# Kernel optimization log

Measured on AMD Instinct MI355X. Metric: run time of the kernel, lower is better.

## Reference

```python
import jax, jax.numpy as jnp
import numpy as np

T, B, F = 160, 640, 40          # time-major input [T, B, F]
H, PJ, L = 768, 256, 3          # nb_hidden, nb_proj, nb_layers
FORGET_BIAS = 1.0               # TF LSTMCell default


def _glorot(k, shape):
    std = (2.0 / (shape[0] + shape[1])) ** 0.5
    return jax.random.normal(k, shape, jnp.float32) * std


def setup_inputs() -> dict:
    key = jax.random.key(0)
    ks = jax.random.split(key, 7)
    x = jax.random.normal(ks[0], (T, B, F), jnp.float32)
    # layer 0: input dim F + proj state PJ; layers 1,2: input dim PJ + PJ
    W0 = _glorot(ks[1], (F + PJ, 4 * H)); b0 = jnp.zeros((4 * H,), jnp.float32)
    P0 = _glorot(ks[2], (H, PJ))
    W1 = _glorot(ks[3], (PJ + PJ, 4 * H)); b1 = jnp.zeros((4 * H,), jnp.float32)
    P1 = _glorot(ks[4], (H, PJ))
    W2 = _glorot(ks[5], (PJ + PJ, 4 * H)); b2 = jnp.zeros((4 * H,), jnp.float32)
    P2 = _glorot(ks[6], (H, PJ))
    return {"x": x, "W0": W0, "b0": b0, "P0": P0,
            "W1": W1, "b1": b1, "P1": P1,
            "W2": W2, "b2": b2, "P2": P2}


def _cell(xt, c, h, W, b, P):
    # TF LSTMCell with num_proj: gates on [x, m_prev]; gate order i, j, f, o.
    z = jnp.concatenate([xt, h], axis=-1) @ W + b            # [B, 4H]
    i, j, f, o = jnp.split(z, 4, axis=-1)
    c_new = jax.nn.sigmoid(f + FORGET_BIAS) * c + jax.nn.sigmoid(i) * jnp.tanh(j)
    m = jax.nn.sigmoid(o) * jnp.tanh(c_new)                  # [B, H]
    h_new = m @ P                                            # projected state [B, PJ]
    return c_new, h_new


def reference(x, W0, b0, P0, W1, b1, P1, W2, b2, P2):
    params = ((W0, b0, P0), (W1, b1, P1), (W2, b2, P2))
    Bd = x.shape[1]
    init = tuple((jnp.zeros((Bd, H), x.dtype), jnp.zeros((Bd, PJ), x.dtype))
                 for _ in range(L))

    def step(carry, xt):
        inp = xt
        new = []
        for (c, h), (W, b, P) in zip(carry, params):
            c, h = _cell(inp, c, h, W, b, P)
            new.append((c, h))
            inp = h
        return tuple(new), None

    carry, _ = jax.lax.scan(step, init, x)
    emb = carry[-1][1]                                       # last layer h at final step, [B, PJ]
    # tf.nn.l2_normalize
    return emb / jnp.sqrt(jnp.maximum(jnp.sum(emb * emb, axis=-1, keepdims=True), 1e-12))
```

## Files before the change

kernel.cpp:

```cpp
#include <hip/hip_runtime.h>

#define Bdim 640
#define Hdim 768
#define PJdim 256
#define Tdim 160
#define NSTEP (Tdim + 2)

typedef _Float16 half8 __attribute__((ext_vector_type(8)));
typedef float floatx4 __attribute__((ext_vector_type(4)));

constexpr size_t HB_HALFS = 3ull * Bdim * PJdim;
constexpr size_t ZP_OFF   = HB_HALFS * 2;
constexpr size_t MB_OFF   = ZP_OFF + 256;
constexpr size_t MB_HALFS = 3ull * Bdim * Hdim;
constexpr size_t X_OFF    = MB_OFF + MB_HALFS * 2;
constexpr size_t X_HALFS  = (size_t)Tdim * Bdim * 40;
constexpr size_t W_OFF    = X_OFF + X_HALFS * 2;
constexpr size_t W_HALFS  = 36ull * 131072;
constexpr size_t P_OFF    = W_OFF + W_HALFS * 2;
constexpr size_t P_HALFS  = 3ull * 196608;
constexpr size_t C_OFF    = P_OFF + P_HALFS * 2;
constexpr size_t C_BYTES  = 3ull * Bdim * Hdim * 4;

__device__ __forceinline__ float sigm(float v) { return 1.0f / (1.0f + __expf(-v)); }
__device__ __forceinline__ float tanh_fast(float v) { return 2.0f / (1.0f + __expf(-2.0f * v)) - 1.0f; }

__device__ __forceinline__ void st_coh16b(void* p, _Float16 h) {
    union { _Float16 h; unsigned short u; } cv; cv.h = h;
    __hip_atomic_store((unsigned short*)p, cv.u, __ATOMIC_RELAXED, __HIP_MEMORY_SCOPE_AGENT);
}

__device__ __forceinline__ void pipe_wait(unsigned* c0, unsigned t0, unsigned* c1, unsigned t1)
{
    if (threadIdx.x == 0) {
        if (t0)
            while (__hip_atomic_load(c0, __ATOMIC_RELAXED, __HIP_MEMORY_SCOPE_AGENT) < t0)
                __builtin_amdgcn_s_sleep(1);
        if (c1 && t1)
            while (__hip_atomic_load(c1, __ATOMIC_RELAXED, __HIP_MEMORY_SCOPE_AGENT) < t1)
                __builtin_amdgcn_s_sleep(1);
        __builtin_amdgcn_fence(__ATOMIC_ACQUIRE, "agent");
    }
    __syncthreads();
}

__device__ __forceinline__ void pipe_sig(unsigned* c)
{
    __syncthreads();
    if (threadIdx.x == 0)
        __hip_atomic_fetch_add(c, 1u, __ATOMIC_RELAXED, __HIP_MEMORY_SCOPE_AGENT);
}

__global__ void repack_kernel(const float* __restrict__ x,
                              const float* __restrict__ W0, const float* __restrict__ W1,
                              const float* __restrict__ W2, const float* __restrict__ P0,
                              const float* __restrict__ P1, const float* __restrict__ P2,
                              _Float16* __restrict__ Wfrag, _Float16* __restrict__ Pfrag,
                              _Float16* __restrict__ x16)
{
    size_t idx = (size_t)blockIdx.x * 256 + threadIdx.x;
    if (idx < W_HALFS) {
        int slab = (int)(idx >> 17);
        int l = slab / 12, ht = slab % 12;
        int r  = (int)(idx & 131071);
        int kc = r >> 13;
        int r2 = r & 8191;
        int g  = r2 >> 11;
        int cf = (r2 >> 9) & 3;
        int u  = r2 & 511;
        int lane = u >> 3, e = u & 7;
        int qd = lane >> 4, ln = lane & 15;
        int k   = kc * 32 + qd * 8 + e;
        int col = g * Hdim + ht * 64 + cf * 16 + ln;
        float v;
        if (l == 0)      v = (k < 296) ? W0[(size_t)k * 3072 + col] : 0.0f;
        else if (l == 1) v = W1[(size_t)k * 3072 + col];
        else             v = W2[(size_t)k * 3072 + col];
        Wfrag[idx] = (_Float16)v;
    } else if (idx < W_HALFS + P_HALFS) {
        size_t i = idx - W_HALFS;
        int l = (int)(i / 196608);
        int r = (int)(i % 196608);
        int cq = r / 49152;
        int r2 = r % 49152;
        int kc = r2 / 2048;
        int r3 = r2 & 2047;
        int cgr = r3 >> 9;
        int u  = r3 & 511;
        int lane = u >> 3, e = u & 7;
        int qd = lane >> 4, ln = lane & 15;
        int k  = kc * 32 + qd * 8 + e;
        int pj = cq * 64 + cgr * 16 + ln;
        const float* P = (l == 0) ? P0 : (l == 1) ? P1 : P2;
        Pfrag[i] = (_Float16)P[(size_t)k * PJdim + pj];
    } else if (idx < W_HALFS + P_HALFS + X_HALFS) {
        size_t i = idx - W_HALFS - P_HALFS;
        x16[i] = (_Float16)x[i];
    }
}

__device__ __forceinline__ void gate_step(
    int l, int b0r, int h0, int KC, int t,
    const half8 (&Breg)[16][2], float (&c)[8][2],
    const float (&bia)[2], const float (&bja)[2], const float (&bfa)[2], const float (&boa)[2],
    const _Float16* __restrict__ x16, const _Float16* __restrict__ h16,
    const _Float16* __restrict__ zerop, _Float16* __restrict__ mbuf,
    _Float16* __restrict__ Ast, float* __restrict__ zst, int tid)
{
    const int wv = tid >> 6, lane = tid & 63, qd = lane >> 4, ln = lane & 15;
    const int g = wv >> 1, hh = wv & 1;
    const int qd8 = qd * 8;
    const int rowg = b0r + wv * 16 + ln;

    const _Float16* xt  = x16 + ((size_t)t * Bdim + rowg) * 40;
    const _Float16* h0b = h16 + (size_t)rowg * PJdim - 40;
    const _Float16* lob = (l > 0) ? h16 + ((size_t)(l - 1) * Bdim + rowg) * PJdim : nullptr;
    const _Float16* hib = h16 + ((size_t)l * Bdim + rowg) * PJdim - 256;

    auto srcp = [&](int kc) -> const _Float16* {
        int k = kc * 32 + qd8;
        if (l == 0) return (k < 40) ? xt + k : (k < 296) ? h0b + k : zerop;
        return (k < 256) ? lob + k : hib + k;
    };

    floatx4 acc[8][2];
    const floatx4 fz = {0.f, 0.f, 0.f, 0.f};
#pragma unroll
    for (int i = 0; i < 8; ++i) { acc[i][0] = fz; acc[i][1] = fz; }

    const int CH = KC >> 1;
    uint4 pre0 = *(const uint4*)srcp(0);
    uint4 pre1 = *(const uint4*)srcp(1);
#pragma unroll
    for (int ch = 0; ch < 8; ++ch) {
        if (ch < CH) {
            _Float16* Aw = Ast + (size_t)(ch & 1) * 8192 + wv * 512 + lane * 8;
            *(uint4*)Aw          = pre0;
            *(uint4*)(Aw + 4096) = pre1;
            if (ch + 1 < CH) {
                pre0 = *(const uint4*)srcp(2 * ch + 2);
                pre1 = *(const uint4*)srcp(2 * ch + 3);
            }
            __syncthreads();
            const _Float16* Ab = Ast + (size_t)(ch & 1) * 8192;
#pragma unroll
            for (int sub = 0; sub < 2; ++sub)
#pragma unroll
                for (int rf = 0; rf < 8; ++rf) {
                    half8 af = *(const half8*)(Ab + sub * 4096 + rf * 512 + lane * 8);
                    acc[rf][0] = __builtin_amdgcn_mfma_f32_16x16x32_f16(af, Breg[2 * ch + sub][0], acc[rf][0], 0, 0, 0);
                    acc[rf][1] = __builtin_amdgcn_mfma_f32_16x16x32_f16(af, Breg[2 * ch + sub][1], acc[rf][1], 0, 0, 0);
                }
        }
    }

    const int trow = tid >> 5;
    const int hc0  = (tid * 2) & 63;
#pragma unroll
    for (int rf = 0; rf < 8; ++rf) {
        __syncthreads();
#pragma unroll
        for (int cf = 0; cf < 2; ++cf)
#pragma unroll
            for (int r = 0; r < 4; ++r)
                zst[(qd * 4 + r) * 256 + g * 64 + hh * 32 + cf * 16 + ln] = acc[rf][cf][r];
        __syncthreads();
        _Float16 mh[2];
#pragma unroll
        for (int j = 0; j < 2; ++j) {
            int hc = hc0 + j;
            float zi = zst[trow * 256 + hc]       + bia[j];
            float zj = zst[trow * 256 + 64 + hc]  + bja[j];
            float zf = zst[trow * 256 + 128 + hc] + bfa[j];
            float zo = zst[trow * 256 + 192 + hc] + boa[j];
            float cn = sigm(zf) * c[rf][j] + sigm(zi) * tanh_fast(zj);
            c[rf][j] = cn;
            mh[j] = (_Float16)(sigm(zo) * tanh_fast(cn));
        }
        union { _Float16 h2[2]; unsigned u; } pk;
        pk.h2[0] = mh[0]; pk.h2[1] = mh[1];
        int row_g = b0r + rf * 16 + trow;
        *(unsigned*)(mbuf + ((size_t)l * Bdim + row_g) * Hdim + h0 + hc0) = pk.u;
    }
}

__device__ __forceinline__ void proj_step(
    int l, int b0r, int cq, const half8 (&Preg)[24],
    const _Float16* __restrict__ mbuf, _Float16* __restrict__ h16,
    _Float16* __restrict__ Ast, int tid, bool xstore)
{
    const int wv = tid >> 6, lane = tid & 63, qd = lane >> 4, ln = lane & 15;
    const int rh = wv >> 2, cgi = wv & 3;
    const int rowg = b0r + wv * 16 + ln;
    const _Float16* mrow = mbuf + ((size_t)l * Bdim + rowg) * Hdim + qd * 8;

    floatx4 pacc[4];
    const floatx4 fz = {0.f, 0.f, 0.f, 0.f};
#pragma unroll
    for (int i = 0; i < 4; ++i) pacc[i] = fz;

    uint4 pre0 = *(const uint4*)(mrow);
    uint4 pre1 = *(const uint4*)(mrow + 32);
#pragma unroll
    for (int ch = 0; ch < 12; ++ch) {
        _Float16* Aw = Ast + (size_t)(ch & 1) * 8192 + wv * 512 + lane * 8;
        *(uint4*)Aw          = pre0;
        *(uint4*)(Aw + 4096) = pre1;
        if (ch < 11) {
            pre0 = *(const uint4*)(mrow + (2 * ch + 2) * 32);
            pre1 = *(const uint4*)(mrow + (2 * ch + 3) * 32);
        }
        __syncthreads();
        const _Float16* Ab = Ast + (size_t)(ch & 1) * 8192;
#pragma unroll
        for (int sub = 0; sub < 2; ++sub)
#pragma unroll
            for (int rfl = 0; rfl < 4; ++rfl) {
                half8 af = *(const half8*)(Ab + sub * 4096 + (rh * 4 + rfl) * 512 + lane * 8);
                pacc[rfl] = __builtin_amdgcn_mfma_f32_16x16x32_f16(af, Preg[2 * ch + sub], pacc[rfl], 0, 0, 0);
            }
    }
    if (xstore) {
#pragma unroll
        for (int rfl = 0; rfl < 4; ++rfl)
#pragma unroll
            for (int r = 0; r < 4; ++r) {
                int row = b0r + (rh * 4 + rfl) * 16 + qd * 4 + r;
                st_coh16b(h16 + ((size_t)l * Bdim + row) * PJdim + cq * 64 + cgi * 16 + ln,
                          (_Float16)pacc[rfl][r]);
            }
    } else {
#pragma unroll
        for (int rfl = 0; rfl < 4; ++rfl)
#pragma unroll
            for (int r = 0; r < 4; ++r) {
                int row = b0r + (rh * 4 + rfl) * 16 + qd * 4 + r;
                h16[((size_t)l * Bdim + row) * PJdim + cq * 64 + cgi * 16 + ln] = (_Float16)pacc[rfl][r];
            }
    }
}

__device__ __forceinline__ void load_Breg(const _Float16* __restrict__ Wfrag, int l, int ht,
                                          int wv, int lane, half8 (&Breg)[16][2])
{
    const int g = wv >> 1, hh = wv & 1;
    const _Float16* wslab = Wfrag + ((size_t)(l * 12 + ht)) * 131072;
#pragma unroll
    for (int kc = 0; kc < 16; ++kc)
#pragma unroll
        for (int cf = 0; cf < 2; ++cf)
            Breg[kc][cf] = *(const half8*)(wslab + kc * 8192 + g * 2048 + (hh * 2 + cf) * 512 + lane * 8);
}

__device__ __forceinline__ void load_Preg(const _Float16* __restrict__ Pfrag, int l, int cq,
                                          int wv, int lane, half8 (&Preg)[24])
{
    const int cgi = wv & 3;
    const _Float16* pslab = Pfrag + (size_t)l * 196608 + (size_t)cq * 49152;
#pragma unroll
    for (int kc = 0; kc < 24; ++kc)
        Preg[kc] = *(const half8*)(pslab + kc * 2048 + cgi * 512 + lane * 8);
}

__device__ __forceinline__ void load_bias(const float* __restrict__ bias, int h0, int tid,
                                          float (&bia)[2], float (&bja)[2], float (&bfa)[2], float (&boa)[2])
{
    int hcg = h0 + ((tid * 2) & 63);
#pragma unroll
    for (int j = 0; j < 2; ++j) {
        bia[j] = bias[hcg + j];
        bja[j] = bias[Hdim + hcg + j];
        bfa[j] = bias[2 * Hdim + hcg + j] + 1.0f;
        boa[j] = bias[3 * Hdim + hcg + j];
    }
}

__device__ __forceinline__ void finalize_row(const _Float16* __restrict__ h16,
                                             float* __restrict__ out, int row, int lane)
{
    const _Float16* e = h16 + ((size_t)2 * Bdim + row) * PJdim + lane * 4;
    float v0 = (float)e[0], v1 = (float)e[1], v2 = (float)e[2], v3 = (float)e[3];
    float ss = v0 * v0 + v1 * v1 + v2 * v2 + v3 * v3;
#pragma unroll
    for (int o = 32; o > 0; o >>= 1) ss += __shfl_xor(ss, o, 64);
    float rs = rsqrtf(fmaxf(ss, 1e-12f));
    float4 o4; o4.x = v0 * rs; o4.y = v1 * rs; o4.z = v2 * rs; o4.w = v3 * rs;
    *(float4*)(out + (size_t)row * PJdim + lane * 4) = o4;
}

__global__ __launch_bounds__(512)
void lstm_persist(const _Float16* __restrict__ x16, const _Float16* __restrict__ Wfrag,
                  const _Float16* __restrict__ Pfrag,
                  const float* __restrict__ bias0, const float* __restrict__ bias1,
                  const float* __restrict__ bias2,
                  _Float16* __restrict__ h16, _Float16* __restrict__ mbuf,
                  const _Float16* __restrict__ zerop, float* __restrict__ out,
                  unsigned* __restrict__ flags)
{
    __shared__ __align__(16) _Float16 Ast[2 * 8192];
    __shared__ __align__(16) float zst[16 * 256];

    const int tid = threadIdx.x, bid = blockIdx.x;
    const int wv = tid >> 6, lane = tid & 63;

    const int xcd = bid & 7, slot = bid >> 3;
    const int gid = xcd * 2 + (slot >> 4);
    const int rr  = slot & 15;
    if (gid >= 15) return;
    const int bt2 = gid / 3, l = gid % 3;
    const int b0r = bt2 * 128;

    unsigned* gd = flags + (size_t)gid * 64;
    unsigned* pd = gd + 32;

    if (rr < 12) {
        const int ht = rr, h0 = ht * 64;
        const int KC = (l == 0) ? 10 : 16;
        half8 Breg[16][2];
        load_Breg(Wfrag, l, ht, wv, lane, Breg);
        float bia[2], bja[2], bfa[2], boa[2];
        load_bias((l == 0) ? bias0 : (l == 1) ? bias1 : bias2, h0, tid, bia, bja, bfa, boa);
        float c[8][2];
#pragma unroll
        for (int i = 0; i < 8; ++i) { c[i][0] = 0.f; c[i][1] = 0.f; }
        unsigned* pd_lo = (l > 0) ? flags + (size_t)(gid - 1) * 64 + 32 : nullptr;
        for (int t = 0; t < Tdim; ++t) {
            pipe_wait(pd, 4u * (unsigned)t, pd_lo, (l > 0) ? 4u * (unsigned)(t + 1) : 0u);
            gate_step(l, b0r, h0, KC, t, Breg, c, bia, bja, bfa, boa,
                      x16, h16, zerop, mbuf, Ast, zst, tid);
            pipe_sig(gd);
        }
        if (l == 2 && rr < 8) {
            pipe_wait(pd, 4u * (unsigned)Tdim, nullptr, 0u);
            int row0 = b0r + rr * 16 + wv * 2;
            finalize_row(h16, out, row0, lane);
            finalize_row(h16, out, row0 + 1, lane);
        }
    } else {
        const int cq = rr - 12;
        const bool xstore = ((gid & 1) == 1) && (gid + 1 < 15) && ((gid + 1) % 3 != 0);
        half8 Preg[24];
        load_Preg(Pfrag, l, cq, wv, lane, Preg);
        unsigned* gd_hi = (l < 2) ? flags + (size_t)(gid + 1) * 64 : nullptr;
        for (int t = 0; t < Tdim; ++t) {
            pipe_wait(gd, 12u * (unsigned)(t + 1), gd_hi, (l < 2) ? 12u * (unsigned)t : 0u);
            proj_step(l, b0r, cq, Preg, mbuf, h16, Ast, tid, xstore);
            pipe_sig(pd);
        }
    }
}

__global__ __launch_bounds__(512)
void gate_fb(const _Float16* __restrict__ x16, const _Float16* __restrict__ Wfrag,
             const float* __restrict__ bias0, const float* __restrict__ bias1,
             const float* __restrict__ bias2,
             _Float16* __restrict__ h16, _Float16* __restrict__ mbuf,
             const _Float16* __restrict__ zerop, float* __restrict__ cfb, int s)
{
    __shared__ __align__(16) _Float16 Ast[2 * 8192];
    __shared__ __align__(16) float zst[16 * 256];
    const int tid = threadIdx.x, bid = blockIdx.x;
    const int ht = bid % 12, z = bid / 12, l = z % 3, bt2 = z / 3;
    const int t = s - l;
    if (t < 0 || t >= Tdim) return;
    const int wv = tid >> 6, lane = tid & 63;
    const int b0r = bt2 * 128, h0 = ht * 64;
    const int KC = (l == 0) ? 10 : 16;
    half8 Breg[16][2];
    load_Breg(Wfrag, l, ht, wv, lane, Breg);
    float bia[2], bja[2], bfa[2], boa[2];
    load_bias((l == 0) ? bias0 : (l == 1) ? bias1 : bias2, h0, tid, bia, bja, bfa, boa);
    const int trow = tid >> 5, hc0 = (tid * 2) & 63;
    float c[8][2];
#pragma unroll
    for (int rf = 0; rf < 8; ++rf)
#pragma unroll
        for (int j = 0; j < 2; ++j)
            c[rf][j] = cfb[((size_t)l * Bdim + b0r + rf * 16 + trow) * Hdim + h0 + hc0 + j];
    gate_step(l, b0r, h0, KC, t, Breg, c, bia, bja, bfa, boa, x16, h16, zerop, mbuf, Ast, zst, tid);
#pragma unroll
    for (int rf = 0; rf < 8; ++rf)
#pragma unroll
        for (int j = 0; j < 2; ++j)
            cfb[((size_t)l * Bdim + b0r + rf * 16 + trow) * Hdim + h0 + hc0 + j] = c[rf][j];
}

__global__ __launch_bounds__(512)
void proj_fb(const _Float16* __restrict__ Pfrag, const _Float16* __restrict__ mbuf,
             _Float16* __restrict__ h16, int s)
{
    __shared__ __align__(16) _Float16 Ast[2 * 8192];
    const int tid = threadIdx.x, bid = blockIdx.x;
    const int cq = bid & 3, z = bid >> 2, l = z % 3, bt2 = z / 3;
    const int tp = s - l;
    if (tp < 0 || tp >= Tdim) return;
    const int wv = tid >> 6, lane = tid & 63;
    half8 Preg[24];
    load_Preg(Pfrag, l, cq, wv, lane, Preg);
    proj_step(l, bt2 * 128, cq, Preg, mbuf, h16, Ast, tid, false);
}

__global__ __launch_bounds__(512)
void fin_fb(const _Float16* __restrict__ h16, float* __restrict__ out)
{
    int row = blockIdx.x * 8 + (threadIdx.x >> 6);
    finalize_row(h16, out, row, threadIdx.x & 63);
}

extern "C" void kernel_launch(void* const* d_in, const int* in_sizes, int n_in,
                              void* d_out, int out_size, void* d_ws, size_t ws_size,
                              hipStream_t stream)
{
    (void)in_sizes; (void)n_in; (void)out_size; (void)ws_size;
    const float* x  = (const float*)d_in[0];
    const float* W0 = (const float*)d_in[1];
    const float* b0 = (const float*)d_in[2];
    const float* P0 = (const float*)d_in[3];
    const float* W1 = (const float*)d_in[4];
    const float* b1 = (const float*)d_in[5];
    const float* P1 = (const float*)d_in[6];
    const float* W2 = (const float*)d_in[7];
    const float* b2 = (const float*)d_in[8];
    const float* P2 = (const float*)d_in[9];

    char* ws = (char*)d_ws;
    _Float16* h16   = (_Float16*)(ws);
    _Float16* zerop = (_Float16*)(ws + ZP_OFF);
    _Float16* mbuf  = (_Float16*)(ws + MB_OFF);
    _Float16* x16   = (_Float16*)(ws + X_OFF);
    _Float16* Wfrag = (_Float16*)(ws + W_OFF);
    _Float16* Pfrag = (_Float16*)(ws + P_OFF);
    float*    cfb   = (float*)(ws + C_OFF);
    unsigned* flags = (unsigned*)(ws + C_OFF);
    float*    outp  = (float*)d_out;

    hipMemsetAsync(ws, 0, ZP_OFF + 256, stream);
    hipMemsetAsync(cfb, 0, C_BYTES, stream);

    {
        constexpr size_t total = W_HALFS + P_HALFS + X_HALFS;
        int grid = (int)((total + 255) / 256);
        repack_kernel<<<grid, 256, 0, stream>>>(x, W0, W1, W2, P0, P1, P2, Wfrag, Pfrag, x16);
    }

    int occ = 0;
    hipError_t oe = hipOccupancyMaxActiveBlocksPerMultiprocessor(&occ, lstm_persist, 512, 0);
    bool coop = (oe == hipSuccess && occ >= 1);
    if (coop) {
        void* args[] = { (void*)&x16, (void*)&Wfrag, (void*)&Pfrag,
                         (void*)&b0, (void*)&b1, (void*)&b2,
                         (void*)&h16, (void*)&mbuf, (void*)&zerop, (void*)&outp,
                         (void*)&flags };
        hipError_t le = hipLaunchCooperativeKernel((const void*)lstm_persist,
                                                   dim3(256), dim3(512), args, 0, stream);
        if (le != hipSuccess) { (void)hipGetLastError(); coop = false; }
    }
    if (!coop) {
        for (int s = 0; s < NSTEP; ++s) {
            gate_fb<<<180, 512, 0, stream>>>(x16, Wfrag, b0, b1, b2, h16, mbuf, zerop, cfb, s);
            proj_fb<<<60, 512, 0, stream>>>(Pfrag, mbuf, h16, s);
        }
        fin_fb<<<80, 512, 0, stream>>>(h16, outp);
    }
}
```

Before: 4.766 ms.

## Batch LDS staging into large K chunks and vectorize gate epilogue

The gate and projection GEMM loops now stage eight K-chunks of activations into shared memory at once, instead of double-buffering two chunks per barrier. This cuts the number of __syncthreads per step from about 8–12 down to 2–4. The gate epilogue stages four row-fragments at a time into a larger zst buffer and processes 8 contiguous hidden units per thread with float4 loads. Biases move to shared memory, and mbuf writes become 16-byte stores. The cost is much larger LDS use (about 64KB zst plus 64KB Ast) and more registers held for prefetch, which may reduce occupancy or change the overlap of loads with MFMA.

```diff
diff --git a/kernel.cpp b/kernel.cpp
--- a/kernel.cpp
+++ b/kernel.cpp
@@ -101,11 +101,11 @@
 
 __device__ __forceinline__ void gate_step(
     int l, int b0r, int h0, int KC, int t,
-    const half8 (&Breg)[16][2], float (&c)[8][2],
-    const float (&bia)[2], const float (&bja)[2], const float (&bfa)[2], const float (&boa)[2],
+    const half8 (&Breg)[16][2], float (&c)[2][8],
     const _Float16* __restrict__ x16, const _Float16* __restrict__ h16,
     const _Float16* __restrict__ zerop, _Float16* __restrict__ mbuf,
-    _Float16* __restrict__ Ast, float* __restrict__ zst, int tid)
+    _Float16* __restrict__ Ast, float* __restrict__ zst, const float* __restrict__ bst,
+    int tid)
 {
     const int wv = tid >> 6, lane = tid & 63, qd = lane >> 4, ln = lane & 15;
     const int g = wv >> 1, hh = wv & 1;
@@ -128,59 +128,84 @@
 #pragma unroll
     for (int i = 0; i < 8; ++i) { acc[i][0] = fz; acc[i][1] = fz; }
 
-    const int CH = KC >> 1;
-    uint4 pre0 = *(const uint4*)srcp(0);
-    uint4 pre1 = *(const uint4*)srcp(1);
-#pragma unroll
-    for (int ch = 0; ch < 8; ++ch) {
-        if (ch < CH) {
-            _Float16* Aw = Ast + (size_t)(ch & 1) * 8192 + wv * 512 + lane * 8;
-            *(uint4*)Aw          = pre0;
-            *(uint4*)(Aw + 4096) = pre1;
-            if (ch + 1 < CH) {
-                pre0 = *(const uint4*)srcp(2 * ch + 2);
-                pre1 = *(const uint4*)srcp(2 * ch + 3);
-            }
-            __syncthreads();
-            const _Float16* Ab = Ast + (size_t)(ch & 1) * 8192;
-#pragma unroll
-            for (int sub = 0; sub < 2; ++sub)
-#pragma unroll
-                for (int rf = 0; rf < 8; ++rf) {
-                    half8 af = *(const half8*)(Ab + sub * 4096 + rf * 512 + lane * 8);
-                    acc[rf][0] = __builtin_amdgcn_mfma_f32_16x16x32_f16(af, Breg[2 * ch + sub][0], acc[rf][0], 0, 0, 0);
-                    acc[rf][1] = __builtin_amdgcn_mfma_f32_16x16x32_f16(af, Breg[2 * ch + sub][1], acc[rf][1], 0, 0, 0);
-                }
-        }
-    }
-
-    const int trow = tid >> 5;
-    const int hc0  = (tid * 2) & 63;
-#pragma unroll
-    for (int rf = 0; rf < 8; ++rf) {
+    _Float16* Aw = Ast + wv * 512 + lane * 8;
+
+    uint4 pre[8];
+#pragma unroll
+    for (int kk = 0; kk < 8; ++kk) pre[kk] = *(const uint4*)srcp(kk);
+#pragma unroll
+    for (int kk = 0; kk < 8; ++kk) *(uint4*)(Aw + (size_t)kk * 4096) = pre[kk];
+    const int n1 = KC - 8;
+    uint4 pre2[8];
+#pragma unroll
+    for (int kk = 0; kk < 8; ++kk) if (kk < n1) pre2[kk] = *(const uint4*)srcp(8 + kk);
+    __syncthreads();
+#pragma unroll
+    for (int kk = 0; kk < 8; ++kk) {
+        const _Float16* Ab = Ast + (size_t)kk * 4096;
+#pragma unroll
+        for (int rf = 0; rf < 8; ++rf) {
+            half8 af = *(const half8*)(Ab + rf * 512 + lane * 8);
+            acc[rf][0] = __builtin_amdgcn_mfma_f32_16x16x32_f16(af, Breg[kk][0], acc[rf][0], 0, 0, 0);
+            acc[rf][1] = __builtin_amdgcn_mfma_f32_16x16x32_f16(af, Breg[kk][1], acc[rf][1], 0, 0, 0);
+        }
+    }
+    __syncthreads();
+#pragma unroll
+    for (int kk = 0; kk < 8; ++kk) if (kk < n1) *(uint4*)(Aw + (size_t)kk * 4096) = pre2[kk];
+    __syncthreads();
+#pragma unroll
+    for (int kk = 0; kk < 8; ++kk) if (kk < n1) {
+        const _Float16* Ab = Ast + (size_t)kk * 4096;
+#pragma unroll
+        for (int rf = 0; rf < 8; ++rf) {
+            half8 af = *(const half8*)(Ab + rf * 512 + lane * 8);
+            acc[rf][0] = __builtin_amdgcn_mfma_f32_16x16x32_f16(af, Breg[8 + kk][0], acc[rf][0], 0, 0, 0);
+            acc[rf][1] = __builtin_amdgcn_mfma_f32_16x16x32_f16(af, Breg[8 + kk][1], acc[rf][1], 0, 0, 0);
+        }
+    }
+
+    const int trow = tid >> 3;
+    const int hcb  = (tid & 7) * 8;
+#pragma unroll
+    for (int p = 0; p < 2; ++p) {
         __syncthreads();
 #pragma unroll
-        for (int cf = 0; cf < 2; ++cf)
-#pragma unroll
-            for (int r = 0; r < 4; ++r)
-                zst[(qd * 4 + r) * 256 + g * 64 + hh * 32 + cf * 16 + ln] = acc[rf][cf][r];
+        for (int rq = 0; rq < 4; ++rq) {
+#pragma unroll
+            for (int cf = 0; cf < 2; ++cf)
+#pragma unroll
+                for (int r = 0; r < 4; ++r)
+                    zst[(rq * 16 + qd * 4 + r) * 256 + g * 64 + hh * 32 + cf * 16 + ln]
+                        = acc[p * 4 + rq][cf][r];
+        }
         __syncthreads();
-        _Float16 mh[2];
-#pragma unroll
-        for (int j = 0; j < 2; ++j) {
-            int hc = hc0 + j;
-            float zi = zst[trow * 256 + hc]       + bia[j];
-            float zj = zst[trow * 256 + 64 + hc]  + bja[j];
-            float zf = zst[trow * 256 + 128 + hc] + bfa[j];
-            float zo = zst[trow * 256 + 192 + hc] + boa[j];
-            float cn = sigm(zf) * c[rf][j] + sigm(zi) * tanh_fast(zj);
-            c[rf][j] = cn;
-            mh[j] = (_Float16)(sigm(zo) * tanh_fast(cn));
-        }
-        union { _Float16 h2[2]; unsigned u; } pk;
-        pk.h2[0] = mh[0]; pk.h2[1] = mh[1];
-        int row_g = b0r + rf * 16 + trow;
-        *(unsigned*)(mbuf + ((size_t)l * Bdim + row_g) * Hdim + h0 + hc0) = pk.u;
+        const float* zrow = zst + trow * 256;
+        float zi[8], zj[8], zf[8], zo[8], bi[8], bj[8], bf[8], bo[8];
+        *(float4*)(zi)     = *(const float4*)(zrow + hcb);
+        *(float4*)(zi + 4) = *(const float4*)(zrow + hcb + 4);
+        *(float4*)(zj)     = *(const float4*)(zrow + 64 + hcb);
+        *(float4*)(zj + 4) = *(const float4*)(zrow + 64 + hcb + 4);
+        *(float4*)(zf)     = *(const float4*)(zrow + 128 + hcb);
+        *(float4*)(zf + 4) = *(const float4*)(zrow + 128 + hcb + 4);
+        *(float4*)(zo)     = *(const float4*)(zrow + 192 + hcb);
+        *(float4*)(zo + 4) = *(const float4*)(zrow + 192 + hcb + 4);
+        *(float4*)(bi)     = *(const float4*)(bst + hcb);
+        *(float4*)(bi + 4) = *(const float4*)(bst + hcb + 4);
+        *(float4*)(bj)     = *(const float4*)(bst + 64 + hcb);
+        *(float4*)(bj + 4) = *(const float4*)(bst + 64 + hcb + 4);
+        *(float4*)(bf)     = *(const float4*)(bst + 128 + hcb);
+        *(float4*)(bf + 4) = *(const float4*)(bst + 128 + hcb + 4);
+        *(float4*)(bo)     = *(const float4*)(bst + 192 + hcb);
+        *(float4*)(bo + 4) = *(const float4*)(bst + 192 + hcb + 4);
+        union { _Float16 h[8]; uint4 v; } pk;
+#pragma unroll
+        for (int u = 0; u < 8; ++u) {
+            float cn = sigm(zf[u] + bf[u]) * c[p][u] + sigm(zi[u] + bi[u]) * tanh_fast(zj[u] + bj[u]);
+            c[p][u] = cn;
+            pk.h[u] = (_Float16)(sigm(zo[u] + bo[u]) * tanh_fast(cn));
+        }
+        *(uint4*)(mbuf + ((size_t)l * Bdim + b0r + p * 64 + trow) * Hdim + h0 + hcb) = pk.v;
     }
 }
 
@@ -193,33 +218,59 @@
     const int rh = wv >> 2, cgi = wv & 3;
     const int rowg = b0r + wv * 16 + ln;
     const _Float16* mrow = mbuf + ((size_t)l * Bdim + rowg) * Hdim + qd * 8;
+    _Float16* Aw = Ast + wv * 512 + lane * 8;
 
     floatx4 pacc[4];
     const floatx4 fz = {0.f, 0.f, 0.f, 0.f};
 #pragma unroll
     for (int i = 0; i < 4; ++i) pacc[i] = fz;
 
-    uint4 pre0 = *(const uint4*)(mrow);
-    uint4 pre1 = *(const uint4*)(mrow + 32);
-#pragma unroll
-    for (int ch = 0; ch < 12; ++ch) {
-        _Float16* Aw = Ast + (size_t)(ch & 1) * 8192 + wv * 512 + lane * 8;
-        *(uint4*)Aw          = pre0;
-        *(uint4*)(Aw + 4096) = pre1;
-        if (ch < 11) {
-            pre0 = *(const uint4*)(mrow + (2 * ch + 2) * 32);
-            pre1 = *(const uint4*)(mrow + (2 * ch + 3) * 32);
-        }
-        __syncthreads();
-        const _Float16* Ab = Ast + (size_t)(ch & 1) * 8192;
-#pragma unroll
-        for (int sub = 0; sub < 2; ++sub)
-#pragma unroll
-            for (int rfl = 0; rfl < 4; ++rfl) {
-                half8 af = *(const half8*)(Ab + sub * 4096 + (rh * 4 + rfl) * 512 + lane * 8);
-                pacc[rfl] = __builtin_amdgcn_mfma_f32_16x16x32_f16(af, Preg[2 * ch + sub], pacc[rfl], 0, 0, 0);
-            }
-    }
+    uint4 pa[8], pb[8];
+#pragma unroll
+    for (int kk = 0; kk < 8; ++kk) pa[kk] = *(const uint4*)(mrow + kk * 32);
+#pragma unroll
+    for (int kk = 0; kk < 8; ++kk) *(uint4*)(Aw + (size_t)kk * 4096) = pa[kk];
+#pragma unroll
+    for (int kk = 0; kk < 8; ++kk) pa[kk] = *(const uint4*)(mrow + (8 + kk) * 32);
+    __syncthreads();
+#pragma unroll
+    for (int kk = 0; kk < 8; ++kk) {
+        const _Float16* Ab = Ast + (size_t)kk * 4096;
+#pragma unroll
+        for (int rfl = 0; rfl < 4; ++rfl) {
+            half8 af = *(const half8*)(Ab + (rh * 4 + rfl) * 512 + lane * 8);
+            pacc[rfl] = __builtin_amdgcn_mfma_f32_16x16x32_f16(af, Preg[kk], pacc[rfl], 0, 0, 0);
+        }
+    }
+    __syncthreads();
+#pragma unroll
+    for (int kk = 0; kk < 8; ++kk) *(uint4*)(Aw + (size_t)kk * 4096) = pa[kk];
+#pragma unroll
+    for (int kk = 0; kk < 8; ++kk) pb[kk] = *(const uint4*)(mrow + (16 + kk) * 32);
+    __syncthreads();
+#pragma unroll
+    for (int kk = 0; kk < 8; ++kk) {
+        const _Float16* Ab = Ast + (size_t)kk * 4096;
+#pragma unroll
+        for (int rfl = 0; rfl < 4; ++rfl) {
+            half8 af = *(const half8*)(Ab + (rh * 4 + rfl) * 512 + lane * 8);
+            pacc[rfl] = __builtin_amdgcn_mfma_f32_16x16x32_f16(af, Preg[8 + kk], pacc[rfl], 0, 0, 0);
+        }
+    }
+    __syncthreads();
+#pragma unroll
+    for (int kk = 0; kk < 8; ++kk) *(uint4*)(Aw + (size_t)kk * 4096) = pb[kk];
+    __syncthreads();
+#pragma unroll
+    for (int kk = 0; kk < 8; ++kk) {
+        const _Float16* Ab = Ast + (size_t)kk * 4096;
+#pragma unroll
+        for (int rfl = 0; rfl < 4; ++rfl) {
+            half8 af = *(const half8*)(Ab + (rh * 4 + rfl) * 512 + lane * 8);
+            pacc[rfl] = __builtin_amdgcn_mfma_f32_16x16x32_f16(af, Preg[16 + kk], pacc[rfl], 0, 0, 0);
+        }
+    }
+
     if (xstore) {
 #pragma unroll
         for (int rfl = 0; rfl < 4; ++rfl)
@@ -262,16 +313,12 @@
         Preg[kc] = *(const half8*)(pslab + kc * 2048 + cgi * 512 + lane * 8);
 }
 
-__device__ __forceinline__ void load_bias(const float* __restrict__ bias, int h0, int tid,
-                                          float (&bia)[2], float (&bja)[2], float (&bfa)[2], float (&boa)[2])
-{
-    int hcg = h0 + ((tid * 2) & 63);
-#pragma unroll
-    for (int j = 0; j < 2; ++j) {
-        bia[j] = bias[hcg + j];
-        bja[j] = bias[Hdim + hcg + j];
-        bfa[j] = bias[2 * Hdim + hcg + j] + 1.0f;
-        boa[j] = bias[3 * Hdim + hcg + j];
+__device__ __forceinline__ void load_bst(const float* __restrict__ bias, int h0, int tid,
+                                         float* __restrict__ bst)
+{
+    if (tid < 256) {
+        int gg = tid >> 6, u = tid & 63;
+        bst[tid] = bias[gg * Hdim + h0 + u] + ((gg == 2) ? 1.0f : 0.0f);
     }
 }
 
@@ -297,8 +344,9 @@
                   const _Float16* __restrict__ zerop, float* __restrict__ out,
                   unsigned* __restrict__ flags)
 {
-    __shared__ __align__(16) _Float16 Ast[2 * 8192];
-    __shared__ __align__(16) float zst[16 * 256];
+    __shared__ __align__(16) _Float16 Ast[8 * 4096];
+    __shared__ __align__(16) float zst[64 * 256];
+    __shared__ __align__(16) float bst[256];
 
     const int tid = threadIdx.x, bid = blockIdx.x;
     const int wv = tid >> 6, lane = tid & 63;
@@ -318,16 +366,17 @@
         const int KC = (l == 0) ? 10 : 16;
         half8 Breg[16][2];
         load_Breg(Wfrag, l, ht, wv, lane, Breg);
-        float bia[2], bja[2], bfa[2], boa[2];
-        load_bias((l == 0) ? bias0 : (l == 1) ? bias1 : bias2, h0, tid, bia, bja, bfa, boa);
-        float c[8][2];
-#pragma unroll
-        for (int i = 0; i < 8; ++i) { c[i][0] = 0.f; c[i][1] = 0.f; }
+        load_bst((l == 0) ? bias0 : (l == 1) ? bias1 : bias2, h0, tid, bst);
+        float c[2][8];
+#pragma unroll
+        for (int p = 0; p < 2; ++p)
+#pragma unroll
+            for (int u = 0; u < 8; ++u) c[p][u] = 0.f;
         unsigned* pd_lo = (l > 0) ? flags + (size_t)(gid - 1) * 64 + 32 : nullptr;
         for (int t = 0; t < Tdim; ++t) {
             pipe_wait(pd, 4u * (unsigned)t, pd_lo, (l > 0) ? 4u * (unsigned)(t + 1) : 0u);
-            gate_step(l, b0r, h0, KC, t, Breg, c, bia, bja, bfa, boa,
-                      x16, h16, zerop, mbuf, Ast, zst, tid);
+            gate_step(l, b0r, h0, KC, t, Breg, c,
+                      x16, h16, zerop, mbuf, Ast, zst, bst, tid);
             pipe_sig(gd);
         }
         if (l == 2 && rr < 8) {
@@ -357,8 +406,9 @@
              _Float16* __restrict__ h16, _Float16* __restrict__ mbuf,
              const _Float16* __restrict__ zerop, float* __restrict__ cfb, int s)
 {
-    __shared__ __align__(16) _Float16 Ast[2 * 8192];
-    __shared__ __align__(16) float zst[16 * 256];
+    __shared__ __align__(16) _Float16 Ast[8 * 4096];
+    __shared__ __align__(16) float zst[64 * 256];
+    __shared__ __align__(16) float bst[256];
     const int tid = threadIdx.x, bid = blockIdx.x;
     const int ht = bid % 12, z = bid / 12, l = z % 3, bt2 = z / 3;
     const int t = s - l;
@@ -368,28 +418,27 @@
     const int KC = (l == 0) ? 10 : 16;
     half8 Breg[16][2];
     load_Breg(Wfrag, l, ht, wv, lane, Breg);
-    float bia[2], bja[2], bfa[2], boa[2];
-    load_bias((l == 0) ? bias0 : (l == 1) ? bias1 : bias2, h0, tid, bia, bja, bfa, boa);
-    const int trow = tid >> 5, hc0 = (tid * 2) & 63;
-    float c[8][2];
-#pragma unroll
-    for (int rf = 0; rf < 8; ++rf)
-#pragma unroll
-        for (int j = 0; j < 2; ++j)
-            c[rf][j] = cfb[((size_t)l * Bdim + b0r + rf * 16 + trow) * Hdim + h0 + hc0 + j];
-    gate_step(l, b0r, h0, KC, t, Breg, c, bia, bja, bfa, boa, x16, h16, zerop, mbuf, Ast, zst, tid);
-#pragma unroll
-    for (int rf = 0; rf < 8; ++rf)
-#pragma unroll
-        for (int j = 0; j < 2; ++j)
-            cfb[((size_t)l * Bdim + b0r + rf * 16 + trow) * Hdim + h0 + hc0 + j] = c[rf][j];
+    load_bst((l == 0) ? bias0 : (l == 1) ? bias1 : bias2, h0, tid, bst);
+    const int trow = tid >> 3, hcb = (tid & 7) * 8;
+    float c[2][8];
+#pragma unroll
+    for (int p = 0; p < 2; ++p)
+#pragma unroll
+        for (int u = 0; u < 8; ++u)
+            c[p][u] = cfb[((size_t)l * Bdim + b0r + p * 64 + trow) * Hdim + h0 + hcb + u];
+    gate_step(l, b0r, h0, KC, t, Breg, c, x16, h16, zerop, mbuf, Ast, zst, bst, tid);
+#pragma unroll
+    for (int p = 0; p < 2; ++p)
+#pragma unroll
+        for (int u = 0; u < 8; ++u)
+            cfb[((size_t)l * Bdim + b0r + p * 64 + trow) * Hdim + h0 + hcb + u] = c[p][u];
 }
 
 __global__ __launch_bounds__(512)
 void proj_fb(const _Float16* __restrict__ Pfrag, const _Float16* __restrict__ mbuf,
              _Float16* __restrict__ h16, int s)
 {
-    __shared__ __align__(16) _Float16 Ast[2 * 8192];
+    __shared__ __align__(16) _Float16 Ast[8 * 4096];
     const int tid = threadIdx.x, bid = blockIdx.x;
     const int cq = bid & 3, z = bid >> 2, l = z % 3, bt2 = z / 3;
     const int tp = s - l;
```

Result: slower. 7.442 ms (+56.2%).
